# Performance work log

Hardware: AMD Instinct MI355X
Metric: run time of the kernel (lower is better)

The kernel has to match this reference:

```python
import jax, jax.numpy as jnp
import numpy as np

S, B, D, H, DFF = 1024, 4, 1024, 16, 4096
HD = D // H
EPS = 1e-5


def setup_inputs() -> dict:
    key = jax.random.key(0)
    ks = jax.random.split(key, 16)

    def w(k, shape):
        return jax.random.normal(k, shape, jnp.float32) * 0.02

    inp = {
        "input": jax.random.normal(ks[0], (S, B, D), jnp.float32),  # [seq, batch, d_model]
        "enc": jax.random.normal(ks[1], (S, B, D), jnp.float32),
    }
    i = 2
    for pfx in ("sa", "ca"):
        for name in ("wq", "wk", "wv", "wo"):
            inp[f"{pfx}_{name}"] = w(ks[i], (D, D)); i += 1
            inp[f"{pfx}_b{name[1]}"] = jnp.zeros((D,), jnp.float32)
    inp["w1"] = w(ks[i], (DFF, D)); i += 1
    inp["b1"] = jnp.zeros((DFF,), jnp.float32)
    inp["w2"] = w(ks[i], (D, DFF)); i += 1
    inp["b2"] = jnp.zeros((D,), jnp.float32)
    for n in (1, 2, 3):
        inp[f"ln{n}_g"] = jnp.ones((D,), jnp.float32)
        inp[f"ln{n}_b"] = jnp.zeros((D,), jnp.float32)
    return inp


def _layernorm(x, g, b):
    m = x.mean(-1, keepdims=True)
    v = x.var(-1, keepdims=True)
    return (x - m) * jax.lax.rsqrt(v + EPS) * g + b


def _mha(query, key, value, wq, bq, wk, bk, wv, bv, wo, bo):
    # query/key/value: [seq, batch, d_model] (seq-first layout)
    def proj(x, w, b):
        y = x @ w.T + b
        s, bsz, _ = y.shape
        return y.reshape(s, bsz, H, HD)  # [s, b, h, hd]

    q = proj(query, wq, bq)
    k = proj(key, wk, bk)
    v = proj(value, wv, bv)
    scores = jnp.einsum("sbhd,tbhd->bhst", q, k) / (HD ** 0.5)  # [b, h, s_q, s_k]
    p = jax.nn.softmax(scores, axis=-1)
    o = jnp.einsum("bhst,tbhd->sbhd", p, v)  # [s_q, b, h, hd]
    o = o.reshape(o.shape[0], o.shape[1], D)  # heads concatenated along features
    return o @ wo.T + bo  # [s_q, b, d_model]


def reference(input, enc,
              sa_wq, sa_bq, sa_wk, sa_bk, sa_wv, sa_bv, sa_wo, sa_bo,
              ca_wq, ca_bq, ca_wk, ca_bk, ca_wv, ca_bv, ca_wo, ca_bo,
              w1, b1, w2, b2,
              ln1_g, ln1_b, ln2_g, ln2_b, ln3_g, ln3_b):
    # self-attention: attn_in_1(input, input, input) -> q=k=v=input
    out1 = _mha(input, input, input, sa_wq, sa_bq, sa_wk, sa_bk, sa_wv, sa_bv, sa_wo, sa_bo)
    out = _layernorm(input + out1, ln1_g, ln1_b)
    # cross-attention: attn_in_2(out, enc, enc) binds key=out, query=enc, value=enc
    out2 = _mha(enc, out, enc, ca_wq, ca_bq, ca_wk, ca_bk, ca_wv, ca_bv, ca_wo, ca_bo)
    out = _layernorm(out + out2, ln2_g, ln2_b)
    # FFN (dropout is identity at p=0 / eval)
    out3 = jax.nn.relu(out @ w1.T + b1) @ w2.T + b2
    return _layernorm(out + out3, ln3_g, ln3_b)
```

## Files before the change

### kernel.cpp

```cpp
#include <hip/hip_runtime.h>
#include <hip/hip_bf16.h>
#include <cstdint>
#include <cstddef>


typedef __bf16 bf16;
typedef __attribute__((ext_vector_type(8))) __bf16 bf16x8;
typedef __attribute__((ext_vector_type(4))) __bf16 bf16x4;
typedef __attribute__((ext_vector_type(4))) float f32x4;

#define SEQ   1024
#define BATCH 4
#define DMOD  1024
#define NHEAD 16
#define HDIM  64
#define NTOK  (SEQ*BATCH)
#define DFF   4096

#define GLD(gp, lp) __builtin_amdgcn_global_load_lds( \
    (__attribute__((address_space(1))) void*)(gp),    \
    (__attribute__((address_space(3))) void*)(lp), 16, 0, 0)

struct CastSeg { const float* src; bf16* dst; int n4; };
struct CastArgs { CastSeg seg[12]; };

__global__ __launch_bounds__(256) void cast_multi(CastArgs a) {
  CastSeg s = a.seg[blockIdx.y];
  int i = blockIdx.x * 256 + threadIdx.x;
  if (i < s.n4) {
    float4 v = ((const float4*)s.src)[i];
    bf16x4 o; o[0] = (bf16)v.x; o[1] = (bf16)v.y; o[2] = (bf16)v.z; o[3] = (bf16)v.w;
    ((bf16x4*)s.dst)[i] = o;
  }
}

__global__ __launch_bounds__(256) void gemm_nt(
    const bf16* __restrict__ A, const bf16* __restrict__ W,
    const float* __restrict__ b0, const float* __restrict__ b1,
    const float* __restrict__ b2, const float* __restrict__ b3,
    bf16* __restrict__ C, int M, int N, int K, int flags, int kc)
{
  __shared__ bf16 As[128 * 64];
  __shared__ bf16 Bs[128 * 64];
  const int tid  = threadIdx.x;
  const int wave = tid >> 6, lane = tid & 63;
  const int quad = lane >> 4, l16 = lane & 15;

  const int nbx = gridDim.x, nby = gridDim.y, nbz = gridDim.z;
  const int nbyX = nby >> 3;
  const int lin = blockIdx.x + nbx * (blockIdx.y + nby * blockIdx.z);
  const int c = lin & 7;
  int q = lin >> 3;
  const int by = c * nbyX + (q % nbyX); q /= nbyX;
  const int bx = q % nbx; q /= nbx;
  const int bz = q;

  const int m0 = by * 128, n0 = bx * 128;
  const int wm = (wave >> 1) * 64, wn = (wave & 1) * 64;

  f32x4 acc[4][4] = {};

  const int srow8 = lane >> 3;
  const int sg = ((lane & 7) ^ srow8) * 8;
  const int kbeg = bz * kc;
  const bf16* Ap = A + (size_t)(m0 + wave * 32 + srow8) * K + kbeg + sg;
  const bf16* Wp = W + (size_t)(n0 + wave * 32 + srow8) * K + kbeg + sg;
  const size_t rstep8 = (size_t)8 * K;
  bf16* AsW = As + (wave * 32) * 64;
  bf16* BsW = Bs + (wave * 32) * 64;
  const int fsw = l16 & 7;

  for (int k0 = 0; k0 < kc; k0 += 64) {
    __syncthreads();
#pragma unroll
    for (int j = 0; j < 4; ++j) {
      GLD(Ap + j * rstep8 + k0, AsW + j * 8 * 64);
      GLD(Wp + j * rstep8 + k0, BsW + j * 8 * 64);
    }
    __syncthreads();
#pragma unroll
    for (int ks = 0; ks < 2; ++ks) {
      const int g = ((ks * 4 + quad) ^ fsw) * 8;
      bf16x8 wf[4], tf[4];
#pragma unroll
      for (int i = 0; i < 4; ++i)
        wf[i] = *(const bf16x8*)(Bs + (wn + i * 16 + l16) * 64 + g);
#pragma unroll
      for (int i = 0; i < 4; ++i)
        tf[i] = *(const bf16x8*)(As + (wm + i * 16 + l16) * 64 + g);
#pragma unroll
      for (int mi = 0; mi < 4; ++mi)
#pragma unroll
        for (int ni = 0; ni < 4; ++ni)
          acc[mi][ni] = __builtin_amdgcn_mfma_f32_16x16x32_bf16(wf[mi], tf[ni], acc[mi][ni], 0, 0, 0);
    }
  }

  if (nbz > 1) {
    bf16* Cp = C + (size_t)bz * M * N;
#pragma unroll
    for (int ni = 0; ni < 4; ++ni) {
      const size_t rowb = (size_t)(m0 + wm + ni * 16 + l16) * N;
#pragma unroll
      for (int mi = 0; mi < 4; ++mi) {
        const int gf = n0 + wn + mi * 16 + quad * 4;
        bf16x4 o; o[0] = (bf16)acc[mi][ni][0]; o[1] = (bf16)acc[mi][ni][1];
        o[2] = (bf16)acc[mi][ni][2]; o[3] = (bf16)acc[mi][ni][3];
        *(bf16x4*)(Cp + rowb + gf) = o;
      }
    }
    return;
  }

  const float* bp[4] = {b0, b1, b2, b3};
  const bool orelu = flags & 1;
#pragma unroll
  for (int ni = 0; ni < 4; ++ni) {
    const size_t rowb = (size_t)(m0 + wm + ni * 16 + l16) * N;
#pragma unroll
    for (int mi = 0; mi < 4; ++mi) {
      const int gf = n0 + wn + mi * 16 + quad * 4;
      const float4 bi = *(const float4*)(bp[gf >> 10] + (gf & 1023));
      float v0 = acc[mi][ni][0] + bi.x, v1 = acc[mi][ni][1] + bi.y;
      float v2 = acc[mi][ni][2] + bi.z, v3 = acc[mi][ni][3] + bi.w;
      if (orelu) {
        v0 = fmaxf(v0, 0.f); v1 = fmaxf(v1, 0.f);
        v2 = fmaxf(v2, 0.f); v3 = fmaxf(v3, 0.f);
      }
      bf16x4 o; o[0] = (bf16)v0; o[1] = (bf16)v1; o[2] = (bf16)v2; o[3] = (bf16)v3;
      *(bf16x4*)(C + rowb + gf) = o;
    }
  }
}

__global__ __launch_bounds__(256) void gemm_qkv(
    const bf16* __restrict__ x0b, const bf16* __restrict__ encb,
    const bf16* __restrict__ Wqkv, const bf16* __restrict__ Wqv,
    const float* __restrict__ sbq, const float* __restrict__ sbk,
    const float* __restrict__ sbv,
    const float* __restrict__ cbq, const float* __restrict__ cbv,
    bf16* __restrict__ Qs, bf16* __restrict__ Ks, bf16* __restrict__ VTs,
    bf16* __restrict__ Qc, bf16* __restrict__ VTc)
{
  __shared__ bf16 As[128 * 64];
  __shared__ bf16 Bs[128 * 64];
  const int tid  = threadIdx.x;
  const int wave = tid >> 6, lane = tid & 63;
  const int quad = lane >> 4, l16 = lane & 15;

  int id = blockIdx.x, seg, bx, by;
  const bf16 *A, *W;
  if (id < 768) {
    seg = 0; const int c = id & 7, q = id >> 3;
    by = c * 4 + (q & 3); bx = q >> 2;
    A = x0b; W = Wqkv;
  } else {
    id -= 768;
    seg = 1; const int c = id & 7, q = id >> 3;
    by = c * 4 + (q & 3); bx = q >> 2;
    A = encb; W = Wqv;
  }
  const int K = 1024;
  const int m0 = by * 128, n0 = bx * 128;
  const int wm = (wave >> 1) * 64, wn = (wave & 1) * 64;

  f32x4 acc[4][4] = {};
  const int srow8 = lane >> 3;
  const int sg = ((lane & 7) ^ srow8) * 8;
  const bf16* Ap = A + (size_t)(m0 + wave * 32 + srow8) * K + sg;
  const bf16* Wp = W + (size_t)(n0 + wave * 32 + srow8) * K + sg;
  const size_t rstep8 = (size_t)8 * K;
  bf16* AsW = As + (wave * 32) * 64;
  bf16* BsW = Bs + (wave * 32) * 64;
  const int fsw = l16 & 7;

  for (int k0 = 0; k0 < K; k0 += 64) {
    __syncthreads();
#pragma unroll
    for (int j = 0; j < 4; ++j) {
      GLD(Ap + j * rstep8 + k0, AsW + j * 8 * 64);
      GLD(Wp + j * rstep8 + k0, BsW + j * 8 * 64);
    }
    __syncthreads();
#pragma unroll
    for (int ks = 0; ks < 2; ++ks) {
      const int g = ((ks * 4 + quad) ^ fsw) * 8;
      bf16x8 wf[4], tf[4];
#pragma unroll
      for (int i = 0; i < 4; ++i)
        wf[i] = *(const bf16x8*)(Bs + (wn + i * 16 + l16) * 64 + g);
#pragma unroll
      for (int i = 0; i < 4; ++i)
        tf[i] = *(const bf16x8*)(As + (wm + i * 16 + l16) * 64 + g);
#pragma unroll
      for (int mi = 0; mi < 4; ++mi)
#pragma unroll
        for (int ni = 0; ni < 4; ++ni)
          acc[mi][ni] = __builtin_amdgcn_mfma_f32_16x16x32_bf16(wf[mi], tf[ni], acc[mi][ni], 0, 0, 0);
    }
  }

  const int region = n0 >> 10;
  const bool isV = (seg == 0) ? (region == 2) : (region == 1);
#pragma unroll
  for (int ni = 0; ni < 4; ++ni) {
    const int i = m0 + wm + ni * 16 + l16;
#pragma unroll
    for (int mi = 0; mi < 4; ++mi) {
      const int gf = n0 + wn + mi * 16 + quad * 4;
      const int lf = gf & 1023;
      if (!isV) {
        if (region == 0) {
          const float* bq = (seg == 0) ? sbq : cbq;
          const float4 bi = *(const float4*)(bq + lf);
          bf16* dst = ((seg == 0) ? Qs : Qc) + (size_t)i * 1024 + lf;
          bf16x4 o;
          o[0] = (bf16)((acc[mi][ni][0] + bi.x) * 0.125f);
          o[1] = (bf16)((acc[mi][ni][1] + bi.y) * 0.125f);
          o[2] = (bf16)((acc[mi][ni][2] + bi.z) * 0.125f);
          o[3] = (bf16)((acc[mi][ni][3] + bi.w) * 0.125f);
          *(bf16x4*)dst = o;
        } else {
          const float4 bi = *(const float4*)(sbk + lf);
          bf16x4 o;
          o[0] = (bf16)(acc[mi][ni][0] + bi.x);
          o[1] = (bf16)(acc[mi][ni][1] + bi.y);
          o[2] = (bf16)(acc[mi][ni][2] + bi.z);
          o[3] = (bf16)(acc[mi][ni][3] + bi.w);
          *(bf16x4*)(Ks + (size_t)i * 1024 + lf) = o;
        }
      } else {
        const float* bv = (seg == 0) ? sbv : cbv;
        const float4 bi = *(const float4*)(bv + lf);
        const int h = lf >> 6, hd = lf & 63;
        const int b = i & 3, s = i >> 2;
        bf16* dst = ((seg == 0) ? VTs : VTc)
                    + (((size_t)b * 16 + h) * 64 + hd) * 1024 + s;
        dst[0]    = (bf16)(acc[mi][ni][0] + bi.x);
        dst[1024] = (bf16)(acc[mi][ni][1] + bi.y);
        dst[2048] = (bf16)(acc[mi][ni][2] + bi.z);
        dst[3072] = (bf16)(acc[mi][ni][3] + bi.w);
      }
    }
  }
}

__global__ __launch_bounds__(256) void attn_kernel(
    const bf16* __restrict__ Q, const bf16* __restrict__ K,
    const bf16* __restrict__ VT, bf16* __restrict__ O)
{
  __shared__ bf16 Kt[64 * 64];
  __shared__ bf16 Vt[64 * 64];

  const int tid = threadIdx.x, w = tid >> 6, lane = tid & 63;
  const int quad = lane >> 4, l16 = lane & 15;
  const int bh = blockIdx.y, b = bh >> 4;
  const int co = (bh & 15) * HDIM;
  const int sq0 = blockIdx.x * 128 + w * 32;

  bf16x8 qf[2][2];
#pragma unroll
  for (int u = 0; u < 2; ++u) {
    const bf16* qp = Q + ((size_t)(sq0 + u * 16 + l16) * BATCH + b) * 1024 + co + quad * 8;
    qf[u][0] = *(const bf16x8*)qp;
    qf[u][1] = *(const bf16x8*)(qp + 32);
  }

  f32x4 oacc[2][4] = {};
  float lsum[2] = {0.f, 0.f};

  const int srow = lane >> 3;
  const int glog = (lane & 7) ^ srow;
  const int sw = l16 & 7;

  for (int t0 = 0; t0 < SEQ; t0 += 64) {
    __syncthreads();
#pragma unroll
    for (int j = 0; j < 2; ++j) {
      const int slot = j * 32 + w * 8 + srow;
      const int m = slot & 15, half = (slot >> 4) & 1, chunk = slot >> 5;
      const int t = chunk * 32 + 8 * (m >> 2) + 4 * half + (m & 3);
      GLD(K + ((size_t)(t0 + t) * BATCH + b) * 1024 + co + glog * 8,
          Kt + (j * 32 + w * 8) * 64);
      const int hd = j * 32 + w * 8 + srow;
      GLD(VT + ((size_t)bh * HDIM + hd) * SEQ + t0 + glog * 8,
          Vt + (j * 32 + w * 8) * 64);
    }
    __syncthreads();

#pragma unroll
    for (int c = 0; c < 2; ++c) {
      const bf16* k0 = Kt + (c * 32 + l16) * 64;
      const bf16* k1 = Kt + (c * 32 + 16 + l16) * 64;
      const int g0 = (quad ^ sw) * 8;
      const int g1 = ((4 + quad) ^ sw) * 8;
      bf16x8 ka00 = *(const bf16x8*)(k0 + g0);
      bf16x8 ka01 = *(const bf16x8*)(k0 + g1);
      bf16x8 ka10 = *(const bf16x8*)(k1 + g0);
      bf16x8 ka11 = *(const bf16x8*)(k1 + g1);
      bf16x8 vf[4];
#pragma unroll
      for (int nt = 0; nt < 4; ++nt)
        vf[nt] = *(const bf16x8*)(Vt + (nt * 16 + l16) * 64 + (((c * 4 + quad) ^ sw) * 8));
#pragma unroll
      for (int u = 0; u < 2; ++u) {
        f32x4 c0 = {}, c1 = {};
        c0 = __builtin_amdgcn_mfma_f32_16x16x32_bf16(ka00, qf[u][0], c0, 0, 0, 0);
        c0 = __builtin_amdgcn_mfma_f32_16x16x32_bf16(ka01, qf[u][1], c0, 0, 0, 0);
        c1 = __builtin_amdgcn_mfma_f32_16x16x32_bf16(ka10, qf[u][0], c1, 0, 0, 0);
        c1 = __builtin_amdgcn_mfma_f32_16x16x32_bf16(ka11, qf[u][1], c1, 0, 0, 0);
        bf16x8 pf; float ls = 0.f;
#pragma unroll
        for (int r = 0; r < 4; ++r) {
          float p0 = __expf(c0[r]);
          float p1 = __expf(c1[r]);
          ls += p0 + p1;
          pf[r] = (bf16)p0;
          pf[4 + r] = (bf16)p1;
        }
        lsum[u] += ls;
#pragma unroll
        for (int nt = 0; nt < 4; ++nt)
          oacc[u][nt] = __builtin_amdgcn_mfma_f32_16x16x32_bf16(pf, vf[nt], oacc[u][nt], 0, 0, 0);
      }
    }
  }

#pragma unroll
  for (int u = 0; u < 2; ++u) {
    float s = lsum[u];
    s += __shfl_xor(s, 16, 64);
    s += __shfl_xor(s, 32, 64);
#pragma unroll
    for (int r = 0; r < 4; ++r) {
      const float inv = 1.0f / __shfl(s, quad * 4 + r, 64);
      const size_t ro = ((size_t)(sq0 + u * 16 + quad * 4 + r) * BATCH + b) * DMOD + co;
#pragma unroll
      for (int nt = 0; nt < 4; ++nt)
        O[ro + nt * 16 + l16] = (bf16)(oacc[u][nt][r] * inv);
    }
  }
}

__global__ __launch_bounds__(256) void add_ln_red(
    const float* __restrict__ Xa,
    const bf16* __restrict__ p0, const bf16* __restrict__ p1,
    const bf16* __restrict__ p2, const bf16* __restrict__ p3, int np,
    const float* __restrict__ bias,
    const float* __restrict__ g, const float* __restrict__ beta,
    float* __restrict__ outf, bf16* __restrict__ outb)
{
  const int row = blockIdx.x, tid = threadIdx.x;
  const size_t base = (size_t)row * DMOD;
  float4 a = ((const float4*)(Xa + base))[tid];
  bf16x4 q0 = ((const bf16x4*)(p0 + base))[tid];
  bf16x4 q1 = ((const bf16x4*)(p1 + base))[tid];
  float x0 = a.x + (float)q0[0] + (float)q1[0];
  float x1 = a.y + (float)q0[1] + (float)q1[1];
  float x2 = a.z + (float)q0[2] + (float)q1[2];
  float x3 = a.w + (float)q0[3] + (float)q1[3];
  if (np > 2) {
    bf16x4 q2 = ((const bf16x4*)(p2 + base))[tid];
    bf16x4 q3 = ((const bf16x4*)(p3 + base))[tid];
    x0 += (float)q2[0] + (float)q3[0]; x1 += (float)q2[1] + (float)q3[1];
    x2 += (float)q2[2] + (float)q3[2]; x3 += (float)q2[3] + (float)q3[3];
  }
  float4 bi = ((const float4*)bias)[tid];
  x0 += bi.x; x1 += bi.y; x2 += bi.z; x3 += bi.w;

  float s  = x0 + x1 + x2 + x3;
  float s2 = x0 * x0 + x1 * x1 + x2 * x2 + x3 * x3;
#pragma unroll
  for (int m = 1; m < 64; m <<= 1) { s += __shfl_xor(s, m, 64); s2 += __shfl_xor(s2, m, 64); }
  __shared__ float red[8];
  if ((tid & 63) == 0) { red[tid >> 6] = s; red[4 + (tid >> 6)] = s2; }
  __syncthreads();
  s  = red[0] + red[1] + red[2] + red[3];
  s2 = red[4] + red[5] + red[6] + red[7];
  const float mean = s * (1.0f / DMOD);
  const float var  = s2 * (1.0f / DMOD) - mean * mean;
  const float rs   = rsqrtf(var + 1e-5f);
  float4 gv = ((const float4*)g)[tid];
  float4 bv = ((const float4*)beta)[tid];
  float y0 = (x0 - mean) * rs * gv.x + bv.x;
  float y1 = (x1 - mean) * rs * gv.y + bv.y;
  float y2 = (x2 - mean) * rs * gv.z + bv.z;
  float y3 = (x3 - mean) * rs * gv.w + bv.w;
  float4 o; o.x = y0; o.y = y1; o.z = y2; o.w = y3;
  ((float4*)(outf + base))[tid] = o;
  if (outb) {
    bf16x4 ob; ob[0] = (bf16)y0; ob[1] = (bf16)y1; ob[2] = (bf16)y2; ob[3] = (bf16)y3;
    ((bf16x4*)(outb + base))[tid] = ob;
  }
}

__global__ __launch_bounds__(256) void reduce_cast(
    const bf16* __restrict__ p0, const bf16* __restrict__ p1,
    const float* __restrict__ bias, bf16* __restrict__ out)
{
  const int row = blockIdx.x, tid = threadIdx.x;
  const size_t base = (size_t)row * DMOD;
  bf16x4 a = ((const bf16x4*)(p0 + base))[tid];
  bf16x4 b = ((const bf16x4*)(p1 + base))[tid];
  float4 bi = ((const float4*)bias)[tid];
  bf16x4 o;
  o[0] = (bf16)((float)a[0] + (float)b[0] + bi.x);
  o[1] = (bf16)((float)a[1] + (float)b[1] + bi.y);
  o[2] = (bf16)((float)a[2] + (float)b[2] + bi.z);
  o[3] = (bf16)((float)a[3] + (float)b[3] + bi.w);
  ((bf16x4*)(out + base))[tid] = o;
}

extern "C" void kernel_launch(void* const* d_in, const int* in_sizes, int n_in,
                              void* d_out, int out_size, void* d_ws, size_t ws_size,
                              hipStream_t stream)
{
  const float* x0    = (const float*)d_in[0];
  const float* enc   = (const float*)d_in[1];
  const float* sa_wq = (const float*)d_in[2];
  const float* sa_bq = (const float*)d_in[3];
  const float* sa_wk = (const float*)d_in[4];
  const float* sa_bk = (const float*)d_in[5];
  const float* sa_wv = (const float*)d_in[6];
  const float* sa_bv = (const float*)d_in[7];
  const float* sa_wo = (const float*)d_in[8];
  const float* sa_bo = (const float*)d_in[9];
  const float* ca_wq = (const float*)d_in[10];
  const float* ca_bq = (const float*)d_in[11];
  const float* ca_wk = (const float*)d_in[12];
  const float* ca_bk = (const float*)d_in[13];
  const float* ca_wv = (const float*)d_in[14];
  const float* ca_bv = (const float*)d_in[15];
  const float* ca_wo = (const float*)d_in[16];
  const float* ca_bo = (const float*)d_in[17];
  const float* w1    = (const float*)d_in[18];
  const float* b1    = (const float*)d_in[19];
  const float* w2    = (const float*)d_in[20];
  const float* b2    = (const float*)d_in[21];
  const float* ln1g  = (const float*)d_in[22];
  const float* ln1b  = (const float*)d_in[23];
  const float* ln2g  = (const float*)d_in[24];
  const float* ln2b  = (const float*)d_in[25];
  const float* ln3g  = (const float*)d_in[26];
  const float* ln3b  = (const float*)d_in[27];

  char* ws = (char*)d_ws;
  size_t off = 0;
  auto take = [&](size_t bytes) -> char* {
    char* p = ws + off; off += (bytes + 255) & ~(size_t)255; return p;
  };
  const size_t WEL = (size_t)DMOD * DMOD;
  const size_t ACT = (size_t)NTOK * DMOD;
  bf16* Wqkv_s = (bf16*)take(3 * WEL * 2);
  bf16* Wo_s   = (bf16*)take(WEL * 2);
  bf16* Wqv_c  = (bf16*)take(2 * WEL * 2);
  bf16* Wk_c   = (bf16*)take(WEL * 2);
  bf16* Wo_c   = (bf16*)take(WEL * 2);
  bf16* W1b    = (bf16*)take(4 * WEL * 2);
  bf16* W2b    = (bf16*)take(4 * WEL * 2);
  bf16* x0b  = (bf16*)take(ACT * 2);
  bf16* encb = (bf16*)take(ACT * 2);
  bf16* Qs   = (bf16*)take(ACT * 2);
  bf16* Ks   = (bf16*)take(ACT * 2);
  bf16* VTs  = (bf16*)take(ACT * 2);
  bf16* Qc   = (bf16*)take(ACT * 2);
  bf16* VTc  = (bf16*)take(ACT * 2);
  bf16* Kc   = (bf16*)take(ACT * 2);
  bf16* ctx  = (bf16*)take(ACT * 2);
  float* out1f = (float*)take(ACT * 4);
  bf16*  out1b = (bf16*)take(ACT * 2);
  bf16*  Hff   = (bf16*)take((size_t)NTOK * DFF * 2);
  bf16* pA = x0b;  bf16* pB = encb;
  bf16* pC = Qs;   bf16* pD = Ks;
  bf16* f0 = Qs;   bf16* f1 = Ks;  bf16* f2 = VTs;  bf16* f3 = Qc;
  (void)ws_size; (void)in_sizes; (void)n_in; (void)out_size;

  CastArgs cargs;
  const int nw  = (int)(WEL / 4);
  const int ntk = (int)(ACT / 4);
  cargs.seg[0]  = {x0,    x0b,            ntk};
  cargs.seg[1]  = {enc,   encb,           ntk};
  cargs.seg[2]  = {sa_wq, Wqkv_s,         nw};
  cargs.seg[3]  = {sa_wk, Wqkv_s + WEL,   nw};
  cargs.seg[4]  = {sa_wv, Wqkv_s + 2*WEL, nw};
  cargs.seg[5]  = {sa_wo, Wo_s,           nw};
  cargs.seg[6]  = {ca_wq, Wqv_c,          nw};
  cargs.seg[7]  = {ca_wv, Wqv_c + WEL,    nw};
  cargs.seg[8]  = {ca_wk, Wk_c,           nw};
  cargs.seg[9]  = {ca_wo, Wo_c,           nw};
  cargs.seg[10] = {w1,    W1b,            nw * 4};
  cargs.seg[11] = {w2,    W2b,            nw * 4};
  cast_multi<<<dim3((ntk + 255) / 256, 12), 256, 0, stream>>>(cargs);

  auto gemm = [&](const bf16* A, const bf16* Wt,
                  const float* bb0, const float* bb1, const float* bb2, const float* bb3,
                  bf16* Cp, int M, int N, int Kd, int flags, int nz) {
    gemm_nt<<<dim3(N / 128, M / 128, nz), 256, 0, stream>>>(
        A, Wt, bb0, bb1, bb2, bb3, Cp, M, N, Kd, flags, Kd / nz);
  };

  gemm_qkv<<<dim3(1280), 256, 0, stream>>>(
      x0b, encb, Wqkv_s, Wqv_c, sa_bq, sa_bk, sa_bv, ca_bq, ca_bv,
      Qs, Ks, VTs, Qc, VTc);
  attn_kernel<<<dim3(SEQ / 128, BATCH * NHEAD), 256, 0, stream>>>(Qs, Ks, VTs, ctx);
  gemm(ctx, Wo_s, nullptr, nullptr, nullptr, nullptr, pA, NTOK, DMOD, DMOD, 0, 2);
  add_ln_red<<<dim3(NTOK), 256, 0, stream>>>(x0, pA, pB, nullptr, nullptr, 2,
                                             sa_bo, ln1g, ln1b, out1f, out1b);
  gemm(out1b, Wk_c, nullptr, nullptr, nullptr, nullptr, pC, NTOK, DMOD, DMOD, 0, 2);
  reduce_cast<<<dim3(NTOK), 256, 0, stream>>>(pC, pD, ca_bk, Kc);
  attn_kernel<<<dim3(SEQ / 128, BATCH * NHEAD), 256, 0, stream>>>(Qc, Kc, VTc, ctx);
  gemm(ctx, Wo_c, nullptr, nullptr, nullptr, nullptr, pA, NTOK, DMOD, DMOD, 0, 2);
  add_ln_red<<<dim3(NTOK), 256, 0, stream>>>(out1f, pA, pB, nullptr, nullptr, 2,
                                             ca_bo, ln2g, ln2b, out1f, out1b);
  gemm(out1b, W1b, b1, b1 + 1024, b1 + 2048, b1 + 3072, Hff, NTOK, DFF, DMOD, 1, 1);
  gemm(Hff, W2b, nullptr, nullptr, nullptr, nullptr, f0, NTOK, DMOD, DFF, 0, 4);
  add_ln_red<<<dim3(NTOK), 256, 0, stream>>>(out1f, f0, f1, f2, f3, 4,
                                             b2, ln3g, ln3b, (float*)d_out, nullptr);
}
```

Baseline: 494.9 us.

## Double-buffer LDS tiles in GEMM and attention kernels to overlap loads with MFMA

Each of the three main kernels (gemm_nt, gemm_qkv, attn_kernel) now has two LDS buffers. The next K-tile's global-to-LDS loads are issued before computing on the current tile, so memory latency overlaps with MFMA work. The two __syncthreads per iteration become one vmcnt-wait plus barrier per tile. This doubles LDS use per block, which may lower occupancy, and it relies on kc/K being a multiple of 128.

After: 499.0 us. Within noise of the previous version (+0.8%).

```diff
diff --git a/kernel.cpp b/kernel.cpp
--- a/kernel.cpp
+++ b/kernel.cpp
@@ -21,6 +21,12 @@
     (__attribute__((address_space(1))) void*)(gp),    \
     (__attribute__((address_space(3))) void*)(lp), 16, 0, 0)
 
+static __device__ __forceinline__ void pipe_sync() {
+  asm volatile("s_waitcnt vmcnt(0)" ::: "memory");
+  __builtin_amdgcn_s_barrier();
+  asm volatile("" ::: "memory");
+}
+
 struct CastSeg { const float* src; bf16* dst; int n4; };
 struct CastArgs { CastSeg seg[12]; };
 
@@ -40,8 +46,8 @@
     const float* __restrict__ b2, const float* __restrict__ b3,
     bf16* __restrict__ C, int M, int N, int K, int flags, int kc)
 {
-  __shared__ bf16 As[128 * 64];
-  __shared__ bf16 Bs[128 * 64];
+  __shared__ bf16 As[2][128 * 64];
+  __shared__ bf16 Bs[2][128 * 64];
   const int tid  = threadIdx.x;
   const int wave = tid >> 6, lane = tid & 63;
   const int quad = lane >> 4, l16 = lane & 15;
@@ -66,35 +72,50 @@
   const bf16* Ap = A + (size_t)(m0 + wave * 32 + srow8) * K + kbeg + sg;
   const bf16* Wp = W + (size_t)(n0 + wave * 32 + srow8) * K + kbeg + sg;
   const size_t rstep8 = (size_t)8 * K;
-  bf16* AsW = As + (wave * 32) * 64;
-  bf16* BsW = Bs + (wave * 32) * 64;
+  const int woff = (wave * 32) * 64;
   const int fsw = l16 & 7;
 
-  for (int k0 = 0; k0 < kc; k0 += 64) {
-    __syncthreads();
+  auto stage = [&](bf16* AsD, bf16* BsD, int k0) {
 #pragma unroll
     for (int j = 0; j < 4; ++j) {
-      GLD(Ap + j * rstep8 + k0, AsW + j * 8 * 64);
-      GLD(Wp + j * rstep8 + k0, BsW + j * 8 * 64);
-    }
-    __syncthreads();
+      GLD(Ap + j * rstep8 + k0, AsD + woff + j * 8 * 64);
+      GLD(Wp + j * rstep8 + k0, BsD + woff + j * 8 * 64);
+    }
+  };
+  auto compute = [&](const bf16* AsB, const bf16* BsB) {
 #pragma unroll
     for (int ks = 0; ks < 2; ++ks) {
       const int g = ((ks * 4 + quad) ^ fsw) * 8;
       bf16x8 wf[4], tf[4];
 #pragma unroll
       for (int i = 0; i < 4; ++i)
-        wf[i] = *(const bf16x8*)(Bs + (wn + i * 16 + l16) * 64 + g);
+        wf[i] = *(const bf16x8*)(BsB + (wn + i * 16 + l16) * 64 + g);
 #pragma unroll
       for (int i = 0; i < 4; ++i)
-        tf[i] = *(const bf16x8*)(As + (wm + i * 16 + l16) * 64 + g);
+        tf[i] = *(const bf16x8*)(AsB + (wm + i * 16 + l16) * 64 + g);
 #pragma unroll
       for (int mi = 0; mi < 4; ++mi)
 #pragma unroll
         for (int ni = 0; ni < 4; ++ni)
           acc[mi][ni] = __builtin_amdgcn_mfma_f32_16x16x32_bf16(wf[mi], tf[ni], acc[mi][ni], 0, 0, 0);
     }
-  }
+  };
+
+  stage(As[0], Bs[0], 0);
+  pipe_sync();
+  int k0 = 0;
+  for (; k0 < kc - 128; k0 += 128) {
+    stage(As[1], Bs[1], k0 + 64);
+    compute(As[0], Bs[0]);
+    pipe_sync();
+    stage(As[0], Bs[0], k0 + 128);
+    compute(As[1], Bs[1]);
+    pipe_sync();
+  }
+  stage(As[1], Bs[1], k0 + 64);
+  compute(As[0], Bs[0]);
+  pipe_sync();
+  compute(As[1], Bs[1]);
 
   if (nbz > 1) {
     bf16* Cp = C + (size_t)bz * M * N;
@@ -142,8 +163,8 @@
     bf16* __restrict__ Qs, bf16* __restrict__ Ks, bf16* __restrict__ VTs,
     bf16* __restrict__ Qc, bf16* __restrict__ VTc)
 {
-  __shared__ bf16 As[128 * 64];
-  __shared__ bf16 Bs[128 * 64];
+  __shared__ bf16 As[2][128 * 64];
+  __shared__ bf16 Bs[2][128 * 64];
   const int tid  = threadIdx.x;
   const int wave = tid >> 6, lane = tid & 63;
   const int quad = lane >> 4, l16 = lane & 15;
@@ -170,35 +191,50 @@
   const bf16* Ap = A + (size_t)(m0 + wave * 32 + srow8) * K + sg;
   const bf16* Wp = W + (size_t)(n0 + wave * 32 + srow8) * K + sg;
   const size_t rstep8 = (size_t)8 * K;
-  bf16* AsW = As + (wave * 32) * 64;
-  bf16* BsW = Bs + (wave * 32) * 64;
+  const int woff = (wave * 32) * 64;
   const int fsw = l16 & 7;
 
-  for (int k0 = 0; k0 < K; k0 += 64) {
-    __syncthreads();
+  auto stage = [&](bf16* AsD, bf16* BsD, int k0) {
 #pragma unroll
     for (int j = 0; j < 4; ++j) {
-      GLD(Ap + j * rstep8 + k0, AsW + j * 8 * 64);
-      GLD(Wp + j * rstep8 + k0, BsW + j * 8 * 64);
-    }
-    __syncthreads();
+      GLD(Ap + j * rstep8 + k0, AsD + woff + j * 8 * 64);
+      GLD(Wp + j * rstep8 + k0, BsD + woff + j * 8 * 64);
+    }
+  };
+  auto compute = [&](const bf16* AsB, const bf16* BsB) {
 #pragma unroll
     for (int ks = 0; ks < 2; ++ks) {
       const int g = ((ks * 4 + quad) ^ fsw) * 8;
       bf16x8 wf[4], tf[4];
 #pragma unroll
       for (int i = 0; i < 4; ++i)
-        wf[i] = *(const bf16x8*)(Bs + (wn + i * 16 + l16) * 64 + g);
+        wf[i] = *(const bf16x8*)(BsB + (wn + i * 16 + l16) * 64 + g);
 #pragma unroll
       for (int i = 0; i < 4; ++i)
-        tf[i] = *(const bf16x8*)(As + (wm + i * 16 + l16) * 64 + g);
+        tf[i] = *(const bf16x8*)(AsB + (wm + i * 16 + l16) * 64 + g);
 #pragma unroll
       for (int mi = 0; mi < 4; ++mi)
 #pragma unroll
         for (int ni = 0; ni < 4; ++ni)
           acc[mi][ni] = __builtin_amdgcn_mfma_f32_16x16x32_bf16(wf[mi], tf[ni], acc[mi][ni], 0, 0, 0);
     }
-  }
+  };
+
+  stage(As[0], Bs[0], 0);
+  pipe_sync();
+  int k0 = 0;
+  for (; k0 < K - 128; k0 += 128) {
+    stage(As[1], Bs[1], k0 + 64);
+    compute(As[0], Bs[0]);
+    pipe_sync();
+    stage(As[0], Bs[0], k0 + 128);
+    compute(As[1], Bs[1]);
+    pipe_sync();
+  }
+  stage(As[1], Bs[1], k0 + 64);
+  compute(As[0], Bs[0]);
+  pipe_sync();
+  compute(As[1], Bs[1]);
 
   const int region = n0 >> 10;
   const bool isV = (seg == 0) ? (region == 2) : (region == 1);
@@ -249,8 +285,8 @@
     const bf16* __restrict__ Q, const bf16* __restrict__ K,
     const bf16* __restrict__ VT, bf16* __restrict__ O)
 {
-  __shared__ bf16 Kt[64 * 64];
-  __shared__ bf16 Vt[64 * 64];
+  __shared__ bf16 Kt[2][64 * 64];
+  __shared__ bf16 Vt[2][64 * 64];
 
   const int tid = threadIdx.x, w = tid >> 6, lane = tid & 63;
   const int quad = lane >> 4, l16 = lane & 15;
@@ -273,25 +309,25 @@
   const int glog = (lane & 7) ^ srow;
   const int sw = l16 & 7;
 
-  for (int t0 = 0; t0 < SEQ; t0 += 64) {
-    __syncthreads();
+  auto stage = [&](bf16* KtD, bf16* VtD, int t0) {
 #pragma unroll
     for (int j = 0; j < 2; ++j) {
       const int slot = j * 32 + w * 8 + srow;
       const int m = slot & 15, half = (slot >> 4) & 1, chunk = slot >> 5;
       const int t = chunk * 32 + 8 * (m >> 2) + 4 * half + (m & 3);
       GLD(K + ((size_t)(t0 + t) * BATCH + b) * 1024 + co + glog * 8,
-          Kt + (j * 32 + w * 8) * 64);
+          KtD + (j * 32 + w * 8) * 64);
       const int hd = j * 32 + w * 8 + srow;
       GLD(VT + ((size_t)bh * HDIM + hd) * SEQ + t0 + glog * 8,
-          Vt + (j * 32 + w * 8) * 64);
-    }
-    __syncthreads();
-
+          VtD + (j * 32 + w * 8) * 64);
+    }
+  };
+
+  auto compute = [&](const bf16* KtB, const bf16* VtB) {
 #pragma unroll
     for (int c = 0; c < 2; ++c) {
-      const bf16* k0 = Kt + (c * 32 + l16) * 64;
-      const bf16* k1 = Kt + (c * 32 + 16 + l16) * 64;
+      const bf16* k0 = KtB + (c * 32 + l16) * 64;
+      const bf16* k1 = KtB + (c * 32 + 16 + l16) * 64;
       const int g0 = (quad ^ sw) * 8;
       const int g1 = ((4 + quad) ^ sw) * 8;
       bf16x8 ka00 = *(const bf16x8*)(k0 + g0);
@@ -301,7 +337,7 @@
       bf16x8 vf[4];
 #pragma unroll
       for (int nt = 0; nt < 4; ++nt)
-        vf[nt] = *(const bf16x8*)(Vt + (nt * 16 + l16) * 64 + (((c * 4 + quad) ^ sw) * 8));
+        vf[nt] = *(const bf16x8*)(VtB + (nt * 16 + l16) * 64 + (((c * 4 + quad) ^ sw) * 8));
 #pragma unroll
       for (int u = 0; u < 2; ++u) {
         f32x4 c0 = {}, c1 = {};
@@ -324,7 +360,23 @@
           oacc[u][nt] = __builtin_amdgcn_mfma_f32_16x16x32_bf16(pf, vf[nt], oacc[u][nt], 0, 0, 0);
       }
     }
-  }
+  };
+
+  stage(Kt[0], Vt[0], 0);
+  pipe_sync();
+  int t0 = 0;
+  for (; t0 < SEQ - 128; t0 += 128) {
+    stage(Kt[1], Vt[1], t0 + 64);
+    compute(Kt[0], Vt[0]);
+    pipe_sync();
+    stage(Kt[0], Vt[0], t0 + 128);
+    compute(Kt[1], Vt[1]);
+    pipe_sync();
+  }
+  stage(Kt[1], Vt[1], SEQ - 64);
+  compute(Kt[0], Vt[0]);
+  pipe_sync();
+  compute(Kt[1], Vt[1]);
 
 #pragma unroll
   for (int u = 0; u < 2; ++u) {
```
